# Kernel optimization log

Measured on AMD Instinct MI355X. Metric: run time of the kernel, lower is better.

## Reference

```python
import jax, jax.numpy as jnp
import numpy as np

B, S, C, P, E = 8, 16, 32, 64, 768       # batch, max_spans, max_cand, max_prop, emb_dim
M = S * C                                 # bags per batch = 512
L = M * P                                 # triplet ids per batch = 32768
T = 100000                                # triplet vocab size
NE = 1000000                              # num_entities


def setup_inputs() -> dict:
    key = jax.random.key(0)
    k0, k1, k2, k3, k4, k5 = jax.random.split(key, 6)
    span_embs = jax.random.normal(k0, (B, S, E), dtype=jnp.float32)
    triplet_ids_tr = jax.random.randint(k1, (B, L), 0, T, dtype=jnp.int32)
    # uniform bags: bag i covers [i*P, (i+1)*P); offsets must start at 0 (EmbeddingBag)
    offsets_tr = jnp.tile(jnp.arange(M, dtype=jnp.int32) * P, (B, 1))
    attention_tr = jax.random.uniform(k2, (B, L), dtype=jnp.float32)
    qid_inds = jax.random.randint(k3, (B, M), 0, NE + 1, dtype=jnp.int32)
    emb_weight = jax.random.normal(k4, (T, E), dtype=jnp.float32) * 0.02
    span_W = jax.random.normal(k5, (E, 1), dtype=jnp.float32) * 0.02
    span_b = jnp.zeros((1,), dtype=jnp.float32)
    return {"span_embs": span_embs, "triplet_ids_tr": triplet_ids_tr,
            "offsets_tr": offsets_tr, "attention_tr": attention_tr,
            "qid_inds": qid_inds, "emb_weight": emb_weight,
            "span_W": span_W, "span_b": span_b}


def _embedding_bag_sum(ids, offs, w, table):
    # ids,w: [L]; offs: [M] sorted, offs[0]==0 -> sum-pooled bags [M, E]
    pos = jnp.arange(ids.shape[0])
    seg = jnp.searchsorted(offs, pos, side='right') - 1  # bag id per element
    gathered = table[ids] * w[:, None]                    # [L, E]
    return jax.ops.segment_sum(gathered, seg, num_segments=M)


def reference(span_embs, triplet_ids_tr, offsets_tr, attention_tr, qid_inds,
              emb_weight, span_W, span_b):
    span_scores = span_embs @ span_W + span_b              # [B, S, 1]
    # torch repeat(1, max_cand, 1): whole span block tiled C times along dim 1
    exp_emb = jnp.tile(span_embs, (1, C, 1))               # [B, C*S, E]
    kb_embs = jax.vmap(_embedding_bag_sum, in_axes=(0, 0, 0, None))(
        triplet_ids_tr, offsets_tr, attention_tr, emb_weight)  # [B, M, E]
    mult1 = (kb_embs * exp_emb).reshape(B, S, C, E)
    sum1 = jnp.sum(mult1, axis=3)                          # [B, S, C]
    sm1 = jax.nn.softmax(sum1, axis=1)                     # softmax over spans
    mult2 = (span_scores * sm1).reshape(B, S * C)
    cand_scores = jax.nn.softmax(mult2, axis=1)            # [B, M]
    # one-hot matmul == scatter-add of cand scores onto entity ids
    scatter = jax.vmap(lambda q, s: jnp.zeros(NE + 1, dtype=s.dtype).at[q].add(s))(
        qid_inds, cand_scores)                             # [B, NE+1]
    x0 = scatter[:, :-1, None]                             # drop padding entity -> [B, NE, 1]
    return jax.nn.softmax(x0, axis=1)
```

## Files before the change

### kernel.cpp

```cpp
#include <hip/hip_runtime.h>

#define B   8
#define S   16
#define C   32
#define P   64
#define E   768
#define M   512
#define LL  32768
#define NE  1000000

__global__ __launch_bounds__(256) void k1_gather_dot(
    const float* __restrict__ emb,
    const int*   __restrict__ ids,
    const float* __restrict__ att,
    const float* __restrict__ span,
    float*       __restrict__ sum1)
{
    const int seg  = blockIdx.x;
    const int b    = seg >> 9;
    const int m    = seg & 511;
    const int lane = threadIdx.x & 63;
    const int wave = threadIdx.x >> 6;

    const float4* sp = reinterpret_cast<const float4*>(span + (size_t)(b * S + (m & 15)) * E);
    const float4 s0 = sp[lane];
    const float4 s1 = sp[lane + 64];
    const float4 s2 = sp[lane + 128];

    const size_t base = (size_t)b * LL + (size_t)m * P;
    float acc = 0.f;
    #pragma unroll 4
    for (int p = wave; p < P; p += 4) {
        const int   id = ids[base + p];
        const float a  = att[base + p];
        const float4* row = reinterpret_cast<const float4*>(emb + (size_t)id * E);
        const float4 r0 = row[lane];
        const float4 r1 = row[lane + 64];
        const float4 r2 = row[lane + 128];
        float d = r0.x*s0.x + r0.y*s0.y + r0.z*s0.z + r0.w*s0.w
                + r1.x*s1.x + r1.y*s1.y + r1.z*s1.z + r1.w*s1.w
                + r2.x*s2.x + r2.y*s2.y + r2.z*s2.z + r2.w*s2.w;
        acc = fmaf(a, d, acc);
    }
    #pragma unroll
    for (int off = 32; off > 0; off >>= 1)
        acc += __shfl_down(acc, off, 64);

    __shared__ float red[4];
    if (lane == 0) red[wave] = acc;
    __syncthreads();
    if (threadIdx.x == 0)
        sum1[seg] = red[0] + red[1] + red[2] + red[3];
}

__global__ __launch_bounds__(512) void k2_softmax_scatter(
    const float* __restrict__ sum1,
    const float* __restrict__ span,
    const float* __restrict__ spanW,
    const float* __restrict__ spanb,
    const int*   __restrict__ qids,
    float*       __restrict__ out)
{
    const int b = blockIdx.x;
    const int t = threadIdx.x;

    __shared__ float ls[512];
    __shared__ float ss[16];

    {
        const int s = t >> 5, j = t & 31;
        const float* sp = span + (size_t)(b * S + s) * E;
        float partial = 0.f;
        for (int e = j; e < E; e += 32) partial = fmaf(sp[e], spanW[e], partial);
        #pragma unroll
        for (int off = 16; off > 0; off >>= 1) partial += __shfl_down(partial, off, 32);
        if (j == 0) ss[s] = partial + spanb[0];
    }

    const float v = sum1[b * M + t];
    ls[t] = v;
    __syncthreads();

    const int c = t & 31;
    float mx = -1e30f;
    #pragma unroll
    for (int s2 = 0; s2 < S; ++s2) mx = fmaxf(mx, ls[s2 * 32 + c]);
    float den = 0.f;
    #pragma unroll
    for (int s2 = 0; s2 < S; ++s2) den += expf(ls[s2 * 32 + c] - mx);
    const float sm1v = expf(v - mx) / den;
    const float m2   = ss[t >> 5] * sm1v;
    __syncthreads();

    ls[t] = m2; __syncthreads();
    for (int off = 256; off > 0; off >>= 1) {
        if (t < off) ls[t] = fmaxf(ls[t], ls[t + off]);
        __syncthreads();
    }
    const float bigM = ls[0];
    __syncthreads();
    const float ex = expf(m2 - bigM);
    ls[t] = ex; __syncthreads();
    for (int off = 256; off > 0; off >>= 1) {
        if (t < off) ls[t] += ls[t + off];
        __syncthreads();
    }
    const float cand = ex / ls[0];

    const int q = qids[b * M + t];
    if (q < NE) atomicAdd(&out[(size_t)b * NE + q], cand);
}

__global__ __launch_bounds__(512) void k3_denom(
    const int*   __restrict__ qids,
    const float* __restrict__ out,
    float*       __restrict__ invden)
{
    const int b = blockIdx.x;
    const int t = threadIdx.x;
    __shared__ int   q[512];
    __shared__ float red[512];

    q[t] = qids[b * M + t];
    __syncthreads();

    float corr = 0.f;
    const int myq = q[t];
    if (myq < NE) {
        bool owner = true;
        for (int j = 0; j < t; ++j)
            if (q[j] == myq) { owner = false; break; }
        if (owner) corr = expf(out[(size_t)b * NE + myq]) - 1.f;
    }
    red[t] = corr;
    __syncthreads();
    for (int off = 256; off > 0; off >>= 1) {
        if (t < off) red[t] += red[t + off];
        __syncthreads();
    }
    if (t == 0) invden[b] = 1.f / (1.0e6f + red[0]);
}

__global__ __launch_bounds__(256) void k4_finalize(
    float*       __restrict__ out,
    const float* __restrict__ invden)
{
    const int N4 = (B * NE) / 4;
    const int i  = blockIdx.x * blockDim.x + threadIdx.x;
    if (i >= N4) return;
    const int   b   = i / (NE / 4);
    const float inv = invden[b];
    float4* o4 = reinterpret_cast<float4*>(out);
    float4 v = o4[i];
    v.x = expf(v.x) * inv;
    v.y = expf(v.y) * inv;
    v.z = expf(v.z) * inv;
    v.w = expf(v.w) * inv;
    o4[i] = v;
}

extern "C" void kernel_launch(void* const* d_in, const int* in_sizes, int n_in,
                              void* d_out, int out_size, void* d_ws, size_t ws_size,
                              hipStream_t stream)
{
    (void)in_sizes; (void)n_in; (void)out_size; (void)ws_size;

    const float* span_embs = (const float*)d_in[0];
    const int*   ids       = (const int*)  d_in[1];
    const float* att       = (const float*)d_in[3];
    const int*   qids      = (const int*)  d_in[4];
    const float* emb       = (const float*)d_in[5];
    const float* spanW     = (const float*)d_in[6];
    const float* spanb     = (const float*)d_in[7];

    float* out    = (float*)d_out;
    float* sum1   = (float*)d_ws;
    float* invden = sum1 + B * M;

    hipMemsetAsync(d_out, 0, (size_t)B * NE * sizeof(float), stream);

    k1_gather_dot<<<B * M, 256, 0, stream>>>(emb, ids, att, span_embs, sum1);
    k2_softmax_scatter<<<B, 512, 0, stream>>>(sum1, span_embs, spanW, spanb, qids, out);
    k3_denom<<<B, 512, 0, stream>>>(qids, out, invden);
    k4_finalize<<<((B * NE / 4) + 255) / 256, 256, 0, stream>>>(out, invden);
}
```

Baseline: 544.4 us.

## Precompute table-span dot products with bf16 MFMA, fuse softmax/denominator, fill+scatter output

Replaces the per-bag gather of full 768-wide embedding rows with a dense precomputed table of dot products between every vocab row and all 128 span vectors, computed with bf16 MFMA. Each bag then needs only a scalar gather per id. The softmax, duplicate-id handling and denominator are fused into one kernel. The memset, atomic scatter and exp finalize pass are replaced by a constant fill plus a sparse scatter of the precomputed values. This trades a full-table GEMM (100k x 768 x 128) for the random gathers and adds bf16 rounding error in the dot products.

```diff
diff --git a/kernel.cpp b/kernel.cpp
--- a/kernel.cpp
+++ b/kernel.cpp
@@ -8,64 +8,124 @@
 #define M   512
 #define LL  32768
 #define NE  1000000
-
-__global__ __launch_bounds__(256) void k1_gather_dot(
+#define TR  100000
+
+typedef __attribute__((ext_vector_type(8))) short short8;
+typedef __attribute__((ext_vector_type(4))) float f32x4;
+
+__device__ __forceinline__ short f2bf(float x) {
+    unsigned u = __float_as_uint(x);
+    u += 0x7FFFu + ((u >> 16) & 1u);
+    return (short)(u >> 16);
+}
+
+__device__ __forceinline__ short8 pack8(float4 lo, float4 hi) {
+    short8 r;
+    r[0] = f2bf(lo.x); r[1] = f2bf(lo.y); r[2] = f2bf(lo.z); r[3] = f2bf(lo.w);
+    r[4] = f2bf(hi.x); r[5] = f2bf(hi.y); r[6] = f2bf(hi.z); r[7] = f2bf(hi.w);
+    return r;
+}
+
+__global__ __launch_bounds__(256) void k_pre_spanbf(
+    const float* __restrict__ span, short* __restrict__ spanbf)
+{
+    const int i = blockIdx.x * 256 + threadIdx.x;
+    if (i < B * S * E) spanbf[i] = f2bf(span[i]);
+}
+
+__global__ __launch_bounds__(256) void k0_dot_table(
     const float* __restrict__ emb,
+    const short* __restrict__ spanbf,
+    float*       __restrict__ dt)
+{
+    const int wave = threadIdx.x >> 6;
+    const int lane = threadIdx.x & 63;
+    const int mrow = lane & 15;
+    const int kq   = lane >> 4;
+    const int rbase = blockIdx.x * 128 + wave * 32;
+
+    const int r0 = rbase + mrow;
+    const int r1 = r0 + 16;
+    const float* a0p = emb + (size_t)(r0 < TR ? r0 : 0) * E;
+    const float* a1p = emb + (size_t)(r1 < TR ? r1 : 0) * E;
+
+    f32x4 acc[2][8];
+    #pragma unroll
+    for (int i = 0; i < 2; ++i)
+        #pragma unroll
+        for (int j = 0; j < 8; ++j)
+            acc[i][j] = f32x4{0.f, 0.f, 0.f, 0.f};
+
+    for (int k0 = 0; k0 < E; k0 += 32) {
+        const int koff = k0 + kq * 8;
+        const float4 a0lo = *(const float4*)(a0p + koff);
+        const float4 a0hi = *(const float4*)(a0p + koff + 4);
+        const float4 a1lo = *(const float4*)(a1p + koff);
+        const float4 a1hi = *(const float4*)(a1p + koff + 4);
+        const short8 A0 = pack8(a0lo, a0hi);
+        const short8 A1 = pack8(a1lo, a1hi);
+        #pragma unroll
+        for (int ct = 0; ct < 8; ++ct) {
+            const short8 Bf = *(const short8*)(spanbf + (size_t)(ct * 16 + mrow) * E + koff);
+            acc[0][ct] = __builtin_amdgcn_mfma_f32_16x16x32_bf16(A0, Bf, acc[0][ct], 0, 0, 0);
+            acc[1][ct] = __builtin_amdgcn_mfma_f32_16x16x32_bf16(A1, Bf, acc[1][ct], 0, 0, 0);
+        }
+    }
+
+    #pragma unroll
+    for (int rt = 0; rt < 2; ++rt) {
+        const int orow = rbase + rt * 16 + kq * 4;
+        #pragma unroll
+        for (int r = 0; r < 4; ++r) {
+            if (orow + r < TR) {
+                float* o = dt + (size_t)(orow + r) * 128 + mrow;
+                #pragma unroll
+                for (int ct = 0; ct < 8; ++ct) o[ct * 16] = acc[rt][ct][r];
+            }
+        }
+    }
+}
+
+__global__ __launch_bounds__(256) void k1_bagdot(
+    const float* __restrict__ dt,
     const int*   __restrict__ ids,
     const float* __restrict__ att,
-    const float* __restrict__ span,
     float*       __restrict__ sum1)
 {
-    const int seg  = blockIdx.x;
-    const int b    = seg >> 9;
-    const int m    = seg & 511;
+    const int seg  = blockIdx.x * 4 + (threadIdx.x >> 6);
     const int lane = threadIdx.x & 63;
-    const int wave = threadIdx.x >> 6;
-
-    const float4* sp = reinterpret_cast<const float4*>(span + (size_t)(b * S + (m & 15)) * E);
-    const float4 s0 = sp[lane];
-    const float4 s1 = sp[lane + 64];
-    const float4 s2 = sp[lane + 128];
+    const int b = seg >> 9;
+    const int m = seg & 511;
+    const int n = (b << 4) | (m & 15);
 
     const size_t base = (size_t)b * LL + (size_t)m * P;
-    float acc = 0.f;
-    #pragma unroll 4
-    for (int p = wave; p < P; p += 4) {
-        const int   id = ids[base + p];
-        const float a  = att[base + p];
-        const float4* row = reinterpret_cast<const float4*>(emb + (size_t)id * E);
-        const float4 r0 = row[lane];
-        const float4 r1 = row[lane + 64];
-        const float4 r2 = row[lane + 128];
-        float d = r0.x*s0.x + r0.y*s0.y + r0.z*s0.z + r0.w*s0.w
-                + r1.x*s1.x + r1.y*s1.y + r1.z*s1.z + r1.w*s1.w
-                + r2.x*s2.x + r2.y*s2.y + r2.z*s2.z + r2.w*s2.w;
-        acc = fmaf(a, d, acc);
-    }
+    const int   id = ids[base + lane];
+    const float a  = att[base + lane];
+    float v = a * dt[(size_t)id * 128 + n];
+
     #pragma unroll
     for (int off = 32; off > 0; off >>= 1)
-        acc += __shfl_down(acc, off, 64);
-
-    __shared__ float red[4];
-    if (lane == 0) red[wave] = acc;
-    __syncthreads();
-    if (threadIdx.x == 0)
-        sum1[seg] = red[0] + red[1] + red[2] + red[3];
-}
-
-__global__ __launch_bounds__(512) void k2_softmax_scatter(
+        v += __shfl_down(v, off, 64);
+    if (lane == 0) sum1[seg] = v;
+}
+
+__global__ __launch_bounds__(512) void k2_fused(
     const float* __restrict__ sum1,
     const float* __restrict__ span,
     const float* __restrict__ spanW,
     const float* __restrict__ spanb,
     const int*   __restrict__ qids,
-    float*       __restrict__ out)
+    float*       __restrict__ sval,
+    float*       __restrict__ invden)
 {
     const int b = blockIdx.x;
     const int t = threadIdx.x;
 
     __shared__ float ls[512];
+    __shared__ float cs[512];
+    __shared__ int   qs[512];
     __shared__ float ss[16];
+    __shared__ float inv_s;
 
     {
         const int s = t >> 5, j = t & 31;
@@ -79,6 +139,7 @@
 
     const float v = sum1[b * M + t];
     ls[t] = v;
+    qs[t] = qids[b * M + t];
     __syncthreads();
 
     const int c = t & 31;
@@ -88,8 +149,7 @@
     float den = 0.f;
     #pragma unroll
     for (int s2 = 0; s2 < S; ++s2) den += expf(ls[s2 * 32 + c] - mx);
-    const float sm1v = expf(v - mx) / den;
-    const float m2   = ss[t >> 5] * sm1v;
+    const float m2 = ss[t >> 5] * (expf(v - mx) / den);
     __syncthreads();
 
     ls[t] = m2; __syncthreads();
@@ -106,57 +166,55 @@
         __syncthreads();
     }
     const float cand = ex / ls[0];
-
-    const int q = qids[b * M + t];
-    if (q < NE) atomicAdd(&out[(size_t)b * NE + q], cand);
-}
-
-__global__ __launch_bounds__(512) void k3_denom(
-    const int*   __restrict__ qids,
-    const float* __restrict__ out,
-    float*       __restrict__ invden)
-{
-    const int b = blockIdx.x;
-    const int t = threadIdx.x;
-    __shared__ int   q[512];
-    __shared__ float red[512];
-
-    q[t] = qids[b * M + t];
-    __syncthreads();
-
-    float corr = 0.f;
-    const int myq = q[t];
-    if (myq < NE) {
-        bool owner = true;
-        for (int j = 0; j < t; ++j)
-            if (q[j] == myq) { owner = false; break; }
-        if (owner) corr = expf(out[(size_t)b * NE + myq]) - 1.f;
-    }
-    red[t] = corr;
+    __syncthreads();
+
+    cs[t] = cand; __syncthreads();
+
+    const int myq = qs[t];
+    float dsum = 0.f;
+    int first = 512;
+    #pragma unroll 8
+    for (int j = 0; j < 512; ++j) {
+        const bool match = (qs[j] == myq);
+        dsum += match ? cs[j] : 0.f;
+        if (match && j < first) first = j;
+    }
+    const bool owner = (first == t) && (myq < NE);
+    const float ev = owner ? expf(dsum) : 1.f;
+
+    ls[t] = owner ? (ev - 1.f) : 0.f;
     __syncthreads();
     for (int off = 256; off > 0; off >>= 1) {
-        if (t < off) red[t] += red[t + off];
+        if (t < off) ls[t] += ls[t + off];
         __syncthreads();
     }
-    if (t == 0) invden[b] = 1.f / (1.0e6f + red[0]);
-}
-
-__global__ __launch_bounds__(256) void k4_finalize(
-    float*       __restrict__ out,
-    const float* __restrict__ invden)
-{
-    const int N4 = (B * NE) / 4;
-    const int i  = blockIdx.x * blockDim.x + threadIdx.x;
-    if (i >= N4) return;
-    const int   b   = i / (NE / 4);
-    const float inv = invden[b];
-    float4* o4 = reinterpret_cast<float4*>(out);
-    float4 v = o4[i];
-    v.x = expf(v.x) * inv;
-    v.y = expf(v.y) * inv;
-    v.z = expf(v.z) * inv;
-    v.w = expf(v.w) * inv;
-    o4[i] = v;
+    if (t == 0) {
+        const float iv = 1.f / (1.0e6f + ls[0]);
+        invden[b] = iv;
+        inv_s = iv;
+    }
+    __syncthreads();
+
+    sval[b * M + t] = owner ? ev * inv_s : 0.f;
+}
+
+__global__ __launch_bounds__(256) void k3_fill(
+    float* __restrict__ out, const float* __restrict__ invden)
+{
+    const int i = blockIdx.x * 256 + threadIdx.x;
+    if (i >= (B * NE) / 4) return;
+    const float v = invden[i / (NE / 4)];
+    reinterpret_cast<float4*>(out)[i] = make_float4(v, v, v, v);
+}
+
+__global__ __launch_bounds__(512) void k4_scatter(
+    const float* __restrict__ sval, const int* __restrict__ qids,
+    float* __restrict__ out)
+{
+    const int b = blockIdx.x, t = threadIdx.x;
+    const float v = sval[b * M + t];
+    const int   q = qids[b * M + t];
+    if (v > 0.f && q < NE) out[(size_t)b * NE + q] = v;
 }
 
 extern "C" void kernel_launch(void* const* d_in, const int* in_sizes, int n_in,
@@ -173,14 +231,18 @@
     const float* spanW     = (const float*)d_in[6];
     const float* spanb     = (const float*)d_in[7];
 
-    float* out    = (float*)d_out;
-    float* sum1   = (float*)d_ws;
-    float* invden = sum1 + B * M;
-
-    hipMemsetAsync(d_out, 0, (size_t)B * NE * sizeof(float), stream);
-
-    k1_gather_dot<<<B * M, 256, 0, stream>>>(emb, ids, att, span_embs, sum1);
-    k2_softmax_scatter<<<B, 512, 0, stream>>>(sum1, span_embs, spanW, spanb, qids, out);
-    k3_denom<<<B, 512, 0, stream>>>(qids, out, invden);
-    k4_finalize<<<((B * NE / 4) + 255) / 256, 256, 0, stream>>>(out, invden);
-}
+    float* out = (float*)d_out;
+
+    float* dt     = (float*)d_ws;
+    float* sum1   = dt + (size_t)TR * 128;
+    float* sval   = sum1 + B * M;
+    float* invden = sval + B * M;
+    short* spanbf = (short*)(invden + 64);
+
+    k_pre_spanbf<<<(B * S * E + 255) / 256, 256, 0, stream>>>(span_embs, spanbf);
+    k0_dot_table<<<(TR + 127) / 128, 256, 0, stream>>>(emb, spanbf, dt);
+    k1_bagdot<<<(B * M) / 4, 256, 0, stream>>>(dt, ids, att, sum1);
+    k2_fused<<<B, 512, 0, stream>>>(sum1, span_embs, spanW, spanb, qids, sval, invden);
+    k3_fill<<<((B * NE / 4) + 255) / 256, 256, 0, stream>>>(out, invden);
+    k4_scatter<<<B, 512, 0, stream>>>(sval, qids, out);
+}
```

New measurement: 597.7 us. 1.1x slower.
